# Performance work log

Measured on AMD Instinct MI355X. Metric: run time of the kernel, lower is better.

Reference implementation:

```python
import jax, jax.numpy as jnp
import numpy as np
from jax import lax

WINDOW_SIZE = 11
NUM_SCALES = 4
SIGMA = 1.5
C1 = 0.01 ** 2
C2 = 0.03 ** 2
MS_WEIGHTS = (0.0448, 0.2856, 0.3001, 0.2363, 0.1333)


def _gaussian_window(window_size, sigma, channel, dtype):
    coords = jnp.arange(window_size, dtype=jnp.float32) - window_size // 2
    g = jnp.exp(-(coords ** 2) / (2.0 * sigma ** 2))
    g = g / g.sum()
    w2d = jnp.outer(g, g)  # [ws, ws]
    # depthwise kernel: [C, 1, ws, ws] (OIHW with feature_group_count=C)
    return jnp.broadcast_to(w2d, (channel, 1, window_size, window_size)).astype(dtype)


def _depthwise_conv(x, window, pad):
    C = x.shape[1]
    return lax.conv_general_dilated(
        x, window, window_strides=(1, 1), padding=[(pad, pad), (pad, pad)],
        dimension_numbers=('NCHW', 'OIHW', 'NCHW'), feature_group_count=C)


def _avg_pool2(x):
    s = lax.reduce_window(x, jnp.array(0.0, x.dtype), lax.add,
                          (1, 1, 2, 2), (1, 1, 2, 2), 'VALID')
    return s * jnp.asarray(0.25, x.dtype)


def _ssim_single_scale(img1, img2, window):
    pad = WINDOW_SIZE // 2
    mu1 = _depthwise_conv(img1, window, pad)
    mu2 = _depthwise_conv(img2, window, pad)
    mu1_sq = mu1 * mu1
    mu2_sq = mu2 * mu2
    mu1_mu2 = mu1 * mu2
    sigma1_sq = _depthwise_conv(img1 * img1, window, pad) - mu1_sq
    sigma2_sq = _depthwise_conv(img2 * img2, window, pad) - mu2_sq
    sigma12 = _depthwise_conv(img1 * img2, window, pad) - mu1_mu2
    ssim_map = ((2 * mu1_mu2 + C1) * (2 * sigma12 + C2)) / \
               ((mu1_sq + mu2_sq + C1) * (sigma1_sq + sigma2_sq + C2))
    return ssim_map.mean()  # size_average=True


def setup_inputs() -> dict:
    key = jax.random.key(0)
    k1, k2 = jax.random.split(key)
    shape = (16, 3, 512, 512)
    img1 = jax.random.uniform(k1, shape, dtype=jnp.float32)
    img2 = jax.random.uniform(k2, shape, dtype=jnp.float32)
    return {"img1": img1, "img2": img2}


def reference(img1, img2):
    channel = img1.shape[1]
    window = _gaussian_window(WINDOW_SIZE, SIGMA, channel, img1.dtype)
    loss = jnp.asarray(0.0, img1.dtype)
    x1, x2 = img1, img2
    for scale in range(NUM_SCALES):
        if scale > 0:
            x1 = _avg_pool2(x1)
            x2 = _avg_pool2(x2)
        ssim_val = _ssim_single_scale(x1, x2, window)
        w = MS_WEIGHTS[scale] if scale < len(MS_WEIGHTS) else 1.0 / NUM_SCALES
        loss = loss + w * (1.0 - ssim_val)
    return loss
```

## Files before the change

kernel.cpp:

```cpp
#include <hip/hip_runtime.h>

typedef float f2 __attribute__((ext_vector_type(2)));

#define PAD 5
#define WSZ 11

__device__ __forceinline__ float gw(int k) {
    const float G[WSZ] = {
        0.0010283782f, 0.0075987580f, 0.0360007600f, 0.1093607000f,
        0.2130055600f, 0.2660117400f,
        0.2130055600f, 0.1093607000f, 0.0360007600f, 0.0075987580f, 0.0010283782f };
    return G[k];
}

__global__ __launch_bounds__(64) void init_accum_kernel(double* accum) {
    if (threadIdx.x < 4) accum[threadIdx.x] = 0.0;
}

template<int RT, bool PLANAR>
__global__ __launch_bounds__(64, 4) void ssim_scale_kernel(
    const float* __restrict__ img1, const float* __restrict__ img2,
    const f2* __restrict__ pair,
    int H, int W,
    double* __restrict__ accum, int slot,
    f2* __restrict__ pout)
{
    __shared__ f2 st[80];
    const int lane = threadIdx.x;
    const int ox = blockIdx.x * 64;
    const int r0 = blockIdx.y * RT;
    const int z  = blockIdx.z;
    const size_t base = (size_t)z * H * W;

    constexpr int NIT = RT + 10;
    const float C1 = 1e-4f, C2 = 9e-4f;

    const int c0 = ox - PAD + lane;
    const bool m0 = (c0 >= 0) & (c0 < W);
    const int c0c = min(max(c0, 0), W - 1);
    const int c1 = ox + 59 + lane;
    const bool m1 = (lane < 10) & (c1 < W);
    const int c1c = min(c1, W - 1);

    f2 P0a = {0.f, 0.f}, P0b = {0.f, 0.f};
    f2 P1a = {0.f, 0.f}, P1b = {0.f, 0.f};

    auto issue = [&](int y, f2& A, f2& B) {
        int yc = min(max(y, 0), H - 1);
        const size_t roff = base + (size_t)yc * W;
        if (PLANAR) {
            A = (f2){ img1[roff + c0c], img2[roff + c0c] };
            if (lane < 10) B = (f2){ img1[roff + c1c], img2[roff + c1c] };
        } else {
            A = pair[roff + c0c];
            if (lane < 10) B = pair[roff + c1c];
        }
    };

    issue(r0 - PAD + 0, P0a, P0b);
    issue(r0 - PAD + 1, P1a, P1b);

    f2 rmu[12], rsq[12];
    float rxx[12];
    f2 psum = {0.f, 0.f};
    float local = 0.f;
    const f2 zero = {0.f, 0.f};

#pragma clang loop unroll(disable)
    for (int b0 = 0; b0 < NIT; b0 += 12) {
#pragma unroll
        for (int j = 0; j < 12; ++j) {
            const int it = b0 + j;
            if (it < NIT) {
                const int y = r0 - PAD + it;
                const bool yok = (y >= 0) & (y < H);

                f2& ca = (j & 1) ? P1a : P0a;
                f2& cb = (j & 1) ? P1b : P0b;
                f2 wa = (yok & m0) ? ca : zero;
                f2 wb = (yok & m1) ? cb : zero;
                issue(y + 2, ca, cb);

                __builtin_amdgcn_fence(__ATOMIC_ACQ_REL, "wavefront");
                __builtin_amdgcn_wave_barrier();
                st[lane] = wa;
                if (lane < 10) st[64 + lane] = wb;
                __builtin_amdgcn_fence(__ATOMIC_ACQ_REL, "wavefront");
                __builtin_amdgcn_wave_barrier();

                f2 hmu = zero, hsq = zero;
                float hxx = 0.f;
#pragma unroll
                for (int k = 0; k < WSZ; ++k) {
                    f2 p = st[lane + k];
                    hmu += p * gw(k);
                    hsq += (p * p) * gw(k);
                    hxx += (p.x * p.y) * gw(k);
                }
                rmu[it % 12] = hmu;
                rsq[it % 12] = hsq;
                rxx[it % 12] = hxx;

                if (pout != nullptr) {
                    const int yt = it - PAD;
                    if ((yt >= 0) & (yt < RT) & (lane < 32)) {
                        f2 s01 = st[PAD + 2 * lane] + st[PAD + 2 * lane + 1];
                        if ((yt & 1) == 0) {
                            psum = s01;
                        } else {
                            f2 m = (psum + s01) * 0.25f;
                            const int Wo = W >> 1;
                            pout[(size_t)z * (H >> 1) * Wo +
                                 (size_t)((r0 + yt) >> 1) * Wo + (ox >> 1) + lane] = m;
                        }
                    }
                }

                if (it >= 10) {
                    f2 vmu = zero, vsq = zero;
                    float vxx = 0.f;
#pragma unroll
                    for (int k = 0; k < WSZ; ++k) {
                        const int s = (j + 2 + k) % 12;
                        vmu += rmu[s] * gw(k);
                        vsq += rsq[s] * gw(k);
                        vxx += rxx[s] * gw(k);
                    }
                    const float mu1 = vmu.x, mu2 = vmu.y;
                    const float mu11 = mu1 * mu1, mu22 = mu2 * mu2, mu12 = mu1 * mu2;
                    const float sig1 = vsq.x - mu11;
                    const float sig2 = vsq.y - mu22;
                    const float sig12 = vxx - mu12;
                    const float num = (2.f * mu12 + C1) * (2.f * sig12 + C2);
                    const float den = (mu11 + mu22 + C1) * (sig1 + sig2 + C2);
                    local += num * __builtin_amdgcn_rcpf(den);
                }
            }
        }
    }

#pragma unroll
    for (int off = 32; off > 0; off >>= 1) local += __shfl_down(local, off);
    if (lane == 0) atomicAdd(&accum[slot], (double)local);
}

__global__ void finalize_kernel(const double* __restrict__ accum, float* __restrict__ out,
                                double c0, double c1, double c2, double c3)
{
    const double w[4] = {0.0448, 0.2856, 0.3001, 0.2363};
    const double cnt[4] = {c0, c1, c2, c3};
    double loss = 0.0;
#pragma unroll
    for (int s = 0; s < 4; ++s) loss += w[s] * (1.0 - accum[s] / cnt[s]);
    out[0] = (float)loss;
}

extern "C" void kernel_launch(void* const* d_in, const int* in_sizes, int n_in,
                              void* d_out, int out_size, void* d_ws, size_t ws_size,
                              hipStream_t stream) {
    const float* img1 = (const float*)d_in[0];
    const float* img2 = (const float*)d_in[1];
    float* out = (float*)d_out;

    const int H0 = 512, W0 = 512;
    const int NC = in_sizes[0] / (H0 * W0);

    double* accum = (double*)d_ws;
    f2* p1 = (f2*)((char*)d_ws + 64);
    f2* p2 = p1 + (size_t)NC * 256 * 256;
    f2* p3 = p2 + (size_t)NC * 128 * 128;

    init_accum_kernel<<<1, 64, 0, stream>>>(accum);

    ssim_scale_kernel<64, true><<<dim3(8, 8, NC), 64, 0, stream>>>(
        img1, img2, nullptr, 512, 512, accum, 0, p1);
    ssim_scale_kernel<16, false><<<dim3(4, 16, NC), 64, 0, stream>>>(
        nullptr, nullptr, p1, 256, 256, accum, 1, p2);
    ssim_scale_kernel<8, false><<<dim3(2, 16, NC), 64, 0, stream>>>(
        nullptr, nullptr, p2, 128, 128, accum, 2, p3);
    ssim_scale_kernel<8, false><<<dim3(1, 8, NC), 64, 0, stream>>>(
        nullptr, nullptr, p3, 64, 64, accum, 3, nullptr);

    double c0 = (double)NC * 512.0 * 512.0;
    double c1 = (double)NC * 256.0 * 256.0;
    double c2 = (double)NC * 128.0 * 128.0;
    double c3 = (double)NC * 64.0 * 64.0;
    finalize_kernel<<<1, 1, 0, stream>>>(accum, out, c0, c1, c2, c3);
}
```

Baseline: 276.9 us.

## Pack multiple waves per block, triple-buffer row prefetch, double-buffer LDS rows

Each block now holds up to four independent wavefronts, each handling its own 64-column strip with a private shared-memory region. Row loads are prefetched three rows ahead instead of two, and the shared staging row alternates between two buffers. The row tile at the first scale shrinks from 64 to 32, which doubles the vertical grid there, and launch bounds change to 256 threads with 6 blocks per SIMD. The aim is more latency hiding and more resident waves, at the cost of more halo rows re-read per output and more register pressure from the deeper prefetch.

```diff
diff --git a/kernel.cpp b/kernel.cpp
--- a/kernel.cpp
+++ b/kernel.cpp
@@ -18,16 +18,18 @@
 }
 
 template<int RT, bool PLANAR>
-__global__ __launch_bounds__(64, 4) void ssim_scale_kernel(
+__global__ __launch_bounds__(256, 6) void ssim_scale_kernel(
     const float* __restrict__ img1, const float* __restrict__ img2,
     const f2* __restrict__ pair,
     int H, int W,
     double* __restrict__ accum, int slot,
     f2* __restrict__ pout)
 {
-    __shared__ f2 st[80];
-    const int lane = threadIdx.x;
-    const int ox = blockIdx.x * 64;
+    __shared__ f2 st[4][2][96];
+    const int lane = threadIdx.x & 63;
+    const int wave = threadIdx.x >> 6;
+    const int WPB  = blockDim.x >> 6;
+    const int ox = (blockIdx.x * WPB + wave) * 64;
     const int r0 = blockIdx.y * RT;
     const int z  = blockIdx.z;
     const size_t base = (size_t)z * H * W;
@@ -42,23 +44,26 @@
     const bool m1 = (lane < 10) & (c1 < W);
     const int c1c = min(c1, W - 1);
 
-    f2 P0a = {0.f, 0.f}, P0b = {0.f, 0.f};
-    f2 P1a = {0.f, 0.f}, P1b = {0.f, 0.f};
+    f2 Pa[3], Pb[3];
+#pragma unroll
+    for (int s = 0; s < 3; ++s) { Pa[s] = (f2){0.f, 0.f}; Pb[s] = (f2){0.f, 0.f}; }
 
-    auto issue = [&](int y, f2& A, f2& B) {
+    auto issue = [&](int it, int s) {
+        int y = r0 - PAD + it;
         int yc = min(max(y, 0), H - 1);
         const size_t roff = base + (size_t)yc * W;
         if (PLANAR) {
-            A = (f2){ img1[roff + c0c], img2[roff + c0c] };
-            if (lane < 10) B = (f2){ img1[roff + c1c], img2[roff + c1c] };
+            Pa[s] = (f2){ img1[roff + c0c], img2[roff + c0c] };
+            if (lane < 10) Pb[s] = (f2){ img1[roff + c1c], img2[roff + c1c] };
         } else {
-            A = pair[roff + c0c];
-            if (lane < 10) B = pair[roff + c1c];
+            Pa[s] = pair[roff + c0c];
+            if (lane < 10) Pb[s] = pair[roff + c1c];
         }
     };
 
-    issue(r0 - PAD + 0, P0a, P0b);
-    issue(r0 - PAD + 1, P1a, P1b);
+    issue(0, 0);
+    issue(1, 1);
+    issue(2, 2);
 
     f2 rmu[12], rsq[12];
     float rxx[12];
@@ -75,16 +80,17 @@
                 const int y = r0 - PAD + it;
                 const bool yok = (y >= 0) & (y < H);
 
-                f2& ca = (j & 1) ? P1a : P0a;
-                f2& cb = (j & 1) ? P1b : P0b;
-                f2 wa = (yok & m0) ? ca : zero;
-                f2 wb = (yok & m1) ? cb : zero;
-                issue(y + 2, ca, cb);
+                const int s3 = j % 3;
+                f2 wa = (yok & m0) ? Pa[s3] : zero;
+                f2 wb = (yok & m1) ? Pb[s3] : zero;
+                issue(it + 3, s3);
+
+                f2* row = st[wave][j & 1];
 
                 __builtin_amdgcn_fence(__ATOMIC_ACQ_REL, "wavefront");
                 __builtin_amdgcn_wave_barrier();
-                st[lane] = wa;
-                if (lane < 10) st[64 + lane] = wb;
+                row[lane] = wa;
+                if (lane < 10) row[64 + lane] = wb;
                 __builtin_amdgcn_fence(__ATOMIC_ACQ_REL, "wavefront");
                 __builtin_amdgcn_wave_barrier();
 
@@ -92,7 +98,7 @@
                 float hxx = 0.f;
 #pragma unroll
                 for (int k = 0; k < WSZ; ++k) {
-                    f2 p = st[lane + k];
+                    f2 p = row[lane + k];
                     hmu += p * gw(k);
                     hsq += (p * p) * gw(k);
                     hxx += (p.x * p.y) * gw(k);
@@ -104,7 +110,7 @@
                 if (pout != nullptr) {
                     const int yt = it - PAD;
                     if ((yt >= 0) & (yt < RT) & (lane < 32)) {
-                        f2 s01 = st[PAD + 2 * lane] + st[PAD + 2 * lane + 1];
+                        f2 s01 = row[PAD + 2 * lane] + row[PAD + 2 * lane + 1];
                         if ((yt & 1) == 0) {
                             psum = s01;
                         } else {
@@ -172,13 +178,13 @@
 
     init_accum_kernel<<<1, 64, 0, stream>>>(accum);
 
-    ssim_scale_kernel<64, true><<<dim3(8, 8, NC), 64, 0, stream>>>(
+    ssim_scale_kernel<32, true><<<dim3(2, 16, NC), 256, 0, stream>>>(
         img1, img2, nullptr, 512, 512, accum, 0, p1);
-    ssim_scale_kernel<16, false><<<dim3(4, 16, NC), 64, 0, stream>>>(
+    ssim_scale_kernel<16, false><<<dim3(1, 16, NC), 256, 0, stream>>>(
         nullptr, nullptr, p1, 256, 256, accum, 1, p2);
-    ssim_scale_kernel<8, false><<<dim3(2, 16, NC), 64, 0, stream>>>(
+    ssim_scale_kernel<8, false><<<dim3(1, 16, NC), 128, 0, stream>>>(
         nullptr, nullptr, p2, 128, 128, accum, 2, p3);
-    ssim_scale_kernel<8, false><<<dim3(1, 8, NC), 64, 0, stream>>>(
+    ssim_scale_kernel<4, false><<<dim3(1, 16, NC), 64, 0, stream>>>(
         nullptr, nullptr, p3, 64, 64, accum, 3, nullptr);
 
     double c0 = (double)NC * 512.0 * 512.0;
```

After: 595.4 us. 2.15x slower.
